# Kernel optimization log

Hardware: AMD Instinct MI355X
Metric: run time of the kernel (lower is better)

The kernel has to match this reference:

```python
import jax, jax.numpy as jnp
import numpy as np

B, L, D, T, S, K = 16, 4095, 768, 768, 64, 8
H = T // 2  # per-direction GRU hidden


def setup_inputs() -> dict:
    key = jax.random.key(0)
    ks = jax.random.split(key, 16)
    sc = 0.05
    hidden = jax.random.normal(ks[0], (B, L, D), jnp.float32)
    attn_len = jax.random.randint(ks[1], (B,), L // 2, L).astype(jnp.int32)
    span_start = jax.random.randint(ks[2], (B, S), 0, L - 16).astype(jnp.int32)
    span_len = jax.random.randint(ks[3], (B, S), 1, 9).astype(jnp.int32)
    return dict(
        hidden=hidden,
        W_ih_f=jax.random.normal(ks[4], (3 * H, D)) * sc,
        W_hh_f=jax.random.normal(ks[5], (3 * H, H)) * sc,
        b_ih_f=jax.random.normal(ks[6], (3 * H,)) * sc,
        b_hh_f=jax.random.normal(ks[7], (3 * H,)) * sc,
        W_ih_b=jax.random.normal(ks[8], (3 * H, D)) * sc,
        W_hh_b=jax.random.normal(ks[9], (3 * H, H)) * sc,
        b_ih_b=jax.random.normal(ks[10], (3 * H,)) * sc,
        b_hh_b=jax.random.normal(ks[11], (3 * H,)) * sc,
        W_ctx=jax.random.normal(ks[12], (T, D)) * sc,
        b_ctx=jax.random.normal(ks[13], (T,)) * sc,
        W_find=jax.random.normal(ks[14], (1, 2 * T)) * sc,
        attn_len=attn_len,
        span_start=span_start,
        span_len=span_len,
    )


def _gru_dir(x, W_ih, W_hh, b_ih, b_hh, reverse):
    # x: [B, S, D] -> [B, S, H]; torch GRU gate order: r, z, n
    def step(h, xt):
        gi = xt @ W_ih.T + b_ih            # [B, 3H]
        gh = h @ W_hh.T + b_hh
        ir, iz, inn = jnp.split(gi, 3, axis=-1)
        hr, hz, hn = jnp.split(gh, 3, axis=-1)
        r = jax.nn.sigmoid(ir + hr)
        z = jax.nn.sigmoid(iz + hz)
        n = jnp.tanh(inn + r * hn)
        h_new = (1.0 - z) * n + z * h
        return h_new, h_new
    xs = jnp.swapaxes(x, 0, 1)             # [S, B, D]
    h0 = jnp.zeros((x.shape[0], W_hh.shape[1]), x.dtype)
    _, ys = jax.lax.scan(step, h0, xs, reverse=reverse)
    return jnp.swapaxes(ys, 0, 1)          # [B, S, H]


def reference(hidden, W_ih_f, W_hh_f, b_ih_f, b_hh_f, W_ih_b, W_hh_b, b_ih_b, b_hh_b,
              W_ctx, b_ctx, W_find, attn_len, span_start, span_len):
    pos = jnp.arange(L)
    # --- per-span mean pooling (ragged spans, vectorized via masks) ---
    end = span_start + span_len - 1        # inclusive end, as hidden[start:end+1]
    mask = (pos[None, None, :] >= span_start[..., None]) & (pos[None, None, :] <= end[..., None])
    maskf = mask.astype(hidden.dtype)      # [B, S, L]
    cnt = maskf.sum(-1, keepdims=True)
    span_rep = jnp.einsum('bsl,bld->bsd', maskf, hidden) / cnt   # [B, S, D]
    # --- bidirectional GRU over the span sequence ---
    h_f = _gru_dir(span_rep, W_ih_f, W_hh_f, b_ih_f, b_hh_f, reverse=False)
    h_b = _gru_dir(span_rep, W_ih_b, W_hh_b, b_ih_b, b_hh_b, reverse=True)
    rep_ac = jnp.concatenate([h_f, h_b], axis=-1)                # [B, S, T]
    # --- context: mean over valid tokens excluding the last valid token, then linear ---
    n_ctx = (attn_len - 1).astype(hidden.dtype)                  # [B]
    ctx_mask = (pos[None, :] < (attn_len - 1)[:, None]).astype(hidden.dtype)
    ctx = jnp.einsum('bl,bld->bd', ctx_mask, hidden) / n_ctx[:, None]
    rep_context = ctx @ W_ctx.T + b_ctx                          # [B, T]
    # --- findm attention: concat + linear(no bias) + sigmoid + topk + gather ---
    all_reps = jnp.concatenate([rep_ac, rep_context[:, None, :]], axis=1)  # [B, S+1, T]
    wq, wk = W_find[0, :T], W_find[0, T:]
    # sigmoid(W [q; k]) = sigmoid(q.wq + k.wk)
    score = jax.nn.sigmoid((rep_ac @ wq)[:, :, None] + (all_reps @ wk)[:, None, :])  # [B, S, S+1]
    vals, idx = jax.lax.top_k(score, K)                          # [B, S, K]
    v1 = jnp.take_along_axis(all_reps[:, None, :, :], idx[..., None], axis=2)        # [B, S, K, T]
    return rep_ac, rep_context, v1, vals, idx
```

## Files before the change

### kernel.cpp

```cpp
#include <hip/hip_runtime.h>
#include <hip/hip_bf16.h>
#include <math.h>

#define BB 16
#define LL 4095
#define DD 768
#define TT 768
#define SS 64
#define KK 8
#define HH 384
#define G3 1152
#define NWPD 24

__global__ void span_mean_kernel(const float* __restrict__ hidden,
                                 const int* __restrict__ sstart,
                                 const int* __restrict__ slen,
                                 float* __restrict__ span) {
    int bs = blockIdx.x;
    int b = bs >> 6;
    int st = sstart[bs];
    int ln = slen[bs];
    const float* base = hidden + ((size_t)b * LL + st) * DD;
    float inv = 1.0f / (float)ln;
    for (int d = threadIdx.x; d < DD; d += 256) {
        float acc = 0.0f;
        for (int r = 0; r < ln; ++r) acc += base[(size_t)r * DD + d];
        span[(size_t)bs * DD + d] = acc * inv;
    }
}

__global__ void ctx_accum_kernel(const float* __restrict__ hidden,
                                 const int* __restrict__ attn_len,
                                 float* __restrict__ ctx) {
    int b = blockIdx.x, chunk = blockIdx.y;
    int lim = attn_len[b] - 1;
    int l0 = chunk * 128;
    int l1 = min(l0 + 128, lim);
    if (l0 >= l1) return;
    int t = threadIdx.x;
    const float* base = hidden + (size_t)b * LL * DD;
    float a0 = 0.f, a1 = 0.f, a2 = 0.f;
    for (int l = l0; l < l1; ++l) {
        const float* row = base + (size_t)l * DD;
        a0 += row[t]; a1 += row[t + 256]; a2 += row[t + 512];
    }
    atomicAdd(&ctx[b * DD + t], a0);
    atomicAdd(&ctx[b * DD + t + 256], a1);
    atomicAdd(&ctx[b * DD + t + 512], a2);
}

__global__ void repctx_kernel(const float* __restrict__ ctxsum,
                              const int* __restrict__ attn_len,
                              const float* __restrict__ W_ctx,
                              const float* __restrict__ b_ctx,
                              float* __restrict__ out_rc) {
    int b = blockIdx.x;
    int j = blockIdx.y * 256 + threadIdx.x;
    __shared__ float cv[DD];
    float inv = 1.0f / (float)(attn_len[b] - 1);
    for (int d = threadIdx.x; d < DD; d += 256) cv[d] = ctxsum[b * DD + d] * inv;
    __syncthreads();
    const float* wr = W_ctx + (size_t)j * DD;
    float acc = b_ctx[j];
    for (int d = 0; d < DD; ++d) acc += wr[d] * cv[d];
    out_rc[b * TT + j] = acc;
}

__global__ __launch_bounds__(256) void gi_gemm_kernel(
        const float* __restrict__ span,
        const float* __restrict__ Wf, const float* __restrict__ Wb,
        const float* __restrict__ bihf, const float* __restrict__ bhhf,
        const float* __restrict__ bihb, const float* __restrict__ bhhb,
        float* __restrict__ gi) {
    int dir = blockIdx.z;
    const float* W = dir ? Wb : Wf;
    const float* bih = dir ? bihb : bihf;
    const float* bhh = dir ? bhhb : bhhf;
    int m0 = blockIdx.x * 64, n0 = blockIdx.y * 64;
    __shared__ float As[64][17];
    __shared__ float Bs[64][17];
    int t = threadIdx.x, tx = t & 15, ty = t >> 4;
    float acc[4][4] = {{0.f}};
    for (int k0 = 0; k0 < DD; k0 += 16) {
        for (int e = t; e < 1024; e += 256) {
            int r = e >> 4, c = e & 15;
            As[r][c] = span[(size_t)(m0 + r) * DD + k0 + c];
            Bs[r][c] = W[(size_t)(n0 + r) * DD + k0 + c];
        }
        __syncthreads();
#pragma unroll
        for (int kk = 0; kk < 16; ++kk) {
            float a[4], bv[4];
#pragma unroll
            for (int i = 0; i < 4; ++i) a[i] = As[ty * 4 + i][kk];
#pragma unroll
            for (int j = 0; j < 4; ++j) bv[j] = Bs[tx * 4 + j][kk];
#pragma unroll
            for (int i = 0; i < 4; ++i)
#pragma unroll
                for (int j = 0; j < 4; ++j) acc[i][j] += a[i] * bv[j];
        }
        __syncthreads();
    }
#pragma unroll
    for (int i = 0; i < 4; ++i)
#pragma unroll
        for (int j = 0; j < 4; ++j) {
            int m = m0 + ty * 4 + i, n = n0 + tx * 4 + j;
            float v = acc[i][j] + bih[n] + (n < 2 * HH ? bhh[n] : 0.0f);
            gi[((size_t)dir * 1024 + m) * G3 + n] = v;
        }
}

__global__ __launch_bounds__(256, 1) void scan_coop_kernel(
        const float* __restrict__ gi,
        const float* __restrict__ Whf, const float* __restrict__ Whb,
        const float* __restrict__ bhhf, const float* __restrict__ bhhb,
        unsigned long long* __restrict__ hpair,
        float* __restrict__ repac) {
    int wg = blockIdx.x;
    int dir = wg / NWPD;
    int w = wg % NWPD;
    int t = threadIdx.x;
    int kseg = t & 15, i_loc = t >> 4;
    int i_glob = w * 16 + i_loc;
    const float* Wh = dir ? Whb : Whf;

    float4 wr[3][6];
#pragma unroll
    for (int g = 0; g < 3; ++g)
#pragma unroll
        for (int j = 0; j < 6; ++j) {
            wr[g][j] = *(const float4*)(Wh + (size_t)(g * HH + i_glob) * HH + kseg * 4 + 64 * j);
            asm volatile("" : "+v"(wr[g][j].x), "+v"(wr[g][j].y),
                              "+v"(wr[g][j].z), "+v"(wr[g][j].w));
        }
    float bhn = (dir ? bhhb : bhhf)[2 * HH + i_glob];

    __shared__ __align__(16) float hs[6144];
    float4* hs4 = (float4*)hs;

    for (int s = 0; s < 64; ++s) {
        int p = dir ? (63 - s) : s;
        const float* grow = gi + ((size_t)dir * 1024 + kseg * 64 + p) * G3;
        float g_r = grow[i_glob], g_z = grow[HH + i_glob], g_n = grow[2 * HH + i_glob];
        {
            const unsigned long long* src = hpair + (size_t)((s & 1) * 2 + dir) * 6144;
            unsigned int expect = (unsigned int)s;
            unsigned long long vals[24];
            for (;;) {
                bool ok = true;
#pragma unroll
                for (int j = 0; j < 24; ++j) {
                    vals[j] = __hip_atomic_load(src + j * 256 + t,
                                                __ATOMIC_RELAXED, __HIP_MEMORY_SCOPE_AGENT);
                    ok &= ((unsigned int)(vals[j] >> 32) == expect);
                }
                if (ok) break;
                __builtin_amdgcn_s_sleep(1);
            }
#pragma unroll
            for (int j = 0; j < 24; ++j)
                hs[j * 256 + t] = __uint_as_float((unsigned int)vals[j]);
        }
        __syncthreads();
        float pr[16], pz[16], pn[16];
#pragma unroll
        for (int b = 0; b < 16; ++b) {
            float4 hq[6];
#pragma unroll
            for (int j = 0; j < 6; ++j) hq[j] = hs4[b * 96 + kseg + 16 * j];
            float ar = 0.f, az = 0.f, an = 0.f;
#pragma unroll
            for (int j = 0; j < 6; ++j) {
                ar += wr[0][j].x * hq[j].x + wr[0][j].y * hq[j].y + wr[0][j].z * hq[j].z + wr[0][j].w * hq[j].w;
                az += wr[1][j].x * hq[j].x + wr[1][j].y * hq[j].y + wr[1][j].z * hq[j].z + wr[1][j].w * hq[j].w;
                an += wr[2][j].x * hq[j].x + wr[2][j].y * hq[j].y + wr[2][j].z * hq[j].z + wr[2][j].w * hq[j].w;
            }
            pr[b] = ar; pz[b] = az; pn[b] = an;
        }
        float qr[8], qz[8], qn[8];
        {
            const bool hi = (kseg & 8) != 0;
#pragma unroll
            for (int j = 0; j < 8; ++j) {
                float sr_ = hi ? pr[j] : pr[j + 8];
                qr[j] = (hi ? pr[j + 8] : pr[j]) + __shfl_xor(sr_, 8);
                float sz_ = hi ? pz[j] : pz[j + 8];
                qz[j] = (hi ? pz[j + 8] : pz[j]) + __shfl_xor(sz_, 8);
                float sn_ = hi ? pn[j] : pn[j + 8];
                qn[j] = (hi ? pn[j + 8] : pn[j]) + __shfl_xor(sn_, 8);
            }
        }
        float ur[4], uz[4], un[4];
        {
            const bool hi = (kseg & 4) != 0;
#pragma unroll
            for (int j = 0; j < 4; ++j) {
                float sr_ = hi ? qr[j] : qr[j + 4];
                ur[j] = (hi ? qr[j + 4] : qr[j]) + __shfl_xor(sr_, 4);
                float sz_ = hi ? qz[j] : qz[j + 4];
                uz[j] = (hi ? qz[j + 4] : qz[j]) + __shfl_xor(sz_, 4);
                float sn_ = hi ? qn[j] : qn[j + 4];
                un[j] = (hi ? qn[j + 4] : qn[j]) + __shfl_xor(sn_, 4);
            }
        }
        float vr[2], vz[2], vn[2];
        {
            const bool hi = (kseg & 2) != 0;
#pragma unroll
            for (int j = 0; j < 2; ++j) {
                float sr_ = hi ? ur[j] : ur[j + 2];
                vr[j] = (hi ? ur[j + 2] : ur[j]) + __shfl_xor(sr_, 2);
                float sz_ = hi ? uz[j] : uz[j + 2];
                vz[j] = (hi ? uz[j + 2] : uz[j]) + __shfl_xor(sz_, 2);
                float sn_ = hi ? un[j] : un[j + 2];
                vn[j] = (hi ? un[j + 2] : un[j]) + __shfl_xor(sn_, 2);
            }
        }
        float sr, sz, sn;
        {
            const bool hi = (kseg & 1) != 0;
            float sr_ = hi ? vr[0] : vr[1];
            sr = (hi ? vr[1] : vr[0]) + __shfl_xor(sr_, 1);
            float sz_ = hi ? vz[0] : vz[1];
            sz = (hi ? vz[1] : vz[0]) + __shfl_xor(sz_, 1);
            float sn_ = hi ? vn[0] : vn[1];
            sn = (hi ? vn[1] : vn[0]) + __shfl_xor(sn_, 1);
        }
        float r = 1.0f / (1.0f + expf(-(g_r + sr)));
        float z = 1.0f / (1.0f + expf(-(g_z + sz)));
        float n = tanhf(g_n + r * (sn + bhn));
        float hold = hs[kseg * 384 + i_glob];
        float hnew = (1.0f - z) * n + z * hold;
        unsigned long long pv = ((unsigned long long)(unsigned int)(s + 1) << 32)
                              | (unsigned long long)__float_as_uint(hnew);
        __hip_atomic_store(hpair + (size_t)(((s + 1) & 1) * 2 + dir) * 6144 + kseg * 384 + i_glob,
                           pv, __ATOMIC_RELAXED, __HIP_MEMORY_SCOPE_AGENT);
        repac[(size_t)(kseg * 64 + p) * TT + dir * HH + i_glob] = hnew;
        __syncthreads();
    }
}

__global__ void qkv_kernel(const float* __restrict__ repac,
                           const float* __restrict__ repctx,
                           const float* __restrict__ Wfind,
                           float* __restrict__ qv, float* __restrict__ kv) {
    int w = blockIdx.x * 4 + (threadIdx.x >> 6);
    int lane = threadIdx.x & 63;
    const float* row;
    const float* vec;
    float* dst;
    if (w < 1024) {
        row = repac + (size_t)w * TT;
        vec = Wfind;
        dst = qv + w;
    } else {
        int u = w - 1024;
        int b = u / 65, j = u % 65;
        row = (j < 64) ? (repac + (size_t)(b * 64 + j) * TT) : (repctx + (size_t)b * TT);
        vec = Wfind + TT;
        dst = kv + u;
    }
    double acc = 0.0;
    for (int d = lane; d < TT; d += 64) acc += (double)row[d] * (double)vec[d];
#pragma unroll
    for (int off = 32; off > 0; off >>= 1) acc += __shfl_down(acc, off);
    if (lane == 0) *dst = (float)acc;
}

__global__ void topk_kernel(const float* __restrict__ qv,
                            const float* __restrict__ kv,
                            float* __restrict__ vals_out,
                            float* __restrict__ idx_out,
                            int* __restrict__ idxw) {
    int t = threadIdx.x;
    int bs = blockIdx.x * 256 + t;
    int b = bs >> 6;
    int b0 = (blockIdx.x * 256) >> 6;
    __shared__ float kvs[4 * 65];
    for (int e = t; e < 4 * 65; e += 256) kvs[e] = kv[(b0 + e / 65) * 65 + e % 65];
    __syncthreads();
    const float* myk = kvs + (b - b0) * 65;
    float q = qv[bs];
    float sc[65];
#pragma unroll 1
    for (int j = 0; j < 65; ++j) {
        float x = q + myk[j];
        float e = (float)exp(-(double)x);
        sc[j] = 1.0f / (1.0f + e);
    }
    unsigned long long taken = 0ull;
    bool tk64 = false;
    for (int kk = 0; kk < 8; ++kk) {
        float best = -3.0e38f;
        int bj = 0;
        for (int j = 0; j < 65; ++j) {
            bool tkn = (j < 64) ? (((taken >> j) & 1ull) != 0ull) : tk64;
            float v = sc[j];
            if (!tkn && v > best) { best = v; bj = j; }
        }
        if (bj < 64) taken |= (1ull << bj); else tk64 = true;
        vals_out[bs * 8 + kk] = best;
        idx_out[bs * 8 + kk] = (float)bj;
        idxw[bs * 8 + kk] = bj;
    }
}

__global__ void v1_kernel(const float* __restrict__ repac,
                          const float* __restrict__ repctx,
                          const int* __restrict__ idxw,
                          float* __restrict__ v1) {
    int bs = blockIdx.x;
    int b = bs >> 6;
    int t = threadIdx.x;
    for (int kk = 0; kk < 8; ++kk) {
        int j = idxw[bs * 8 + kk];
        const float* src = (j < 64) ? (repac + (size_t)(b * 64 + j) * TT)
                                    : (repctx + (size_t)b * TT);
        float* dst = v1 + ((size_t)bs * 8 + kk) * TT;
        for (int d = t; d < DD; d += 256) dst[d] = src[d];
    }
}

extern "C" void kernel_launch(void* const* d_in, const int* in_sizes, int n_in,
                              void* d_out, int out_size, void* d_ws, size_t ws_size,
                              hipStream_t stream) {
    const float* hidden    = (const float*)d_in[0];
    const float* W_ih_f    = (const float*)d_in[1];
    const float* W_hh_f    = (const float*)d_in[2];
    const float* b_ih_f    = (const float*)d_in[3];
    const float* b_hh_f    = (const float*)d_in[4];
    const float* W_ih_b    = (const float*)d_in[5];
    const float* W_hh_b    = (const float*)d_in[6];
    const float* b_ih_b    = (const float*)d_in[7];
    const float* b_hh_b    = (const float*)d_in[8];
    const float* W_ctx     = (const float*)d_in[9];
    const float* b_ctx     = (const float*)d_in[10];
    const float* W_find    = (const float*)d_in[11];
    const int*   attn_len  = (const int*)d_in[12];
    const int*   span_start= (const int*)d_in[13];
    const int*   span_len  = (const int*)d_in[14];
    (void)in_sizes; (void)n_in; (void)out_size; (void)ws_size;

    float* ws   = (float*)d_ws;
    float* span = ws;
    float* gi   = span + 786432;
    float* ctx  = gi + 2359296;
    float* qv   = ctx + 12288;
    float* kv   = qv + 1024;
    int*   idxw = (int*)(kv + 1040);
    unsigned long long* hpair = (unsigned long long*)span;

    float* out      = (float*)d_out;
    float* o_repac  = out;
    float* o_repctx = out + 786432;
    float* o_v1     = out + 798720;
    float* o_vals   = out + 7090176;
    float* o_idx    = out + 7098368;

    hipMemsetAsync(ctx, 0, (size_t)BB * DD * sizeof(float), stream);

    span_mean_kernel<<<1024, 256, 0, stream>>>(hidden, span_start, span_len, span);
    ctx_accum_kernel<<<dim3(BB, 32), 256, 0, stream>>>(hidden, attn_len, ctx);
    repctx_kernel<<<dim3(BB, 3), 256, 0, stream>>>(ctx, attn_len, W_ctx, b_ctx, o_repctx);
    gi_gemm_kernel<<<dim3(16, 18, 2), 256, 0, stream>>>(span, W_ih_f, W_ih_b,
                                                        b_ih_f, b_hh_f, b_ih_b, b_hh_b, gi);
    hipMemsetAsync(hpair, 0, (size_t)24576 * sizeof(unsigned long long), stream);
    scan_coop_kernel<<<48, 256, 0, stream>>>(gi, W_hh_f, W_hh_b, b_hh_f, b_hh_b,
                                             hpair, o_repac);
    qkv_kernel<<<516, 256, 0, stream>>>(o_repac, o_repctx, W_find, qv, kv);
    topk_kernel<<<4, 256, 0, stream>>>(qv, kv, o_vals, o_idx, idxw);
    v1_kernel<<<1024, 256, 0, stream>>>(o_repac, o_repctx, idxw, o_v1);
}
```

Measured before the change: 947.8 us.

## Double-buffer scan hidden state, skip polling own slice, vectorize gi GEMM smem reads

The GRU scan kernel now keeps two LDS hidden-state buffers. Each workgroup writes its own new h slice straight into the next buffer and skips the global atomic polling for the entries it owns. This removes the trailing __syncthreads per step and cuts global spin-load traffic on the cross-workgroup critical path. Separately, the gi GEMM stores its shared tiles transposed (k-major), so each thread reads a float4 instead of four strided scalar loads. The risks are a race on the double buffer, since its correctness depends on the barrier after polling, and bank conflicts from the transposed tile stores.

```diff
diff --git a/kernel.cpp b/kernel.cpp
--- a/kernel.cpp
+++ b/kernel.cpp
@@ -77,24 +77,23 @@
     const float* bih = dir ? bihb : bihf;
     const float* bhh = dir ? bhhb : bhhf;
     int m0 = blockIdx.x * 64, n0 = blockIdx.y * 64;
-    __shared__ float As[64][17];
-    __shared__ float Bs[64][17];
+    __shared__ float As[16][68];
+    __shared__ float Bs[16][68];
     int t = threadIdx.x, tx = t & 15, ty = t >> 4;
     float acc[4][4] = {{0.f}};
     for (int k0 = 0; k0 < DD; k0 += 16) {
         for (int e = t; e < 1024; e += 256) {
             int r = e >> 4, c = e & 15;
-            As[r][c] = span[(size_t)(m0 + r) * DD + k0 + c];
-            Bs[r][c] = W[(size_t)(n0 + r) * DD + k0 + c];
+            As[c][r] = span[(size_t)(m0 + r) * DD + k0 + c];
+            Bs[c][r] = W[(size_t)(n0 + r) * DD + k0 + c];
         }
         __syncthreads();
 #pragma unroll
         for (int kk = 0; kk < 16; ++kk) {
-            float a[4], bv[4];
-#pragma unroll
-            for (int i = 0; i < 4; ++i) a[i] = As[ty * 4 + i][kk];
-#pragma unroll
-            for (int j = 0; j < 4; ++j) bv[j] = Bs[tx * 4 + j][kk];
+            float4 a4 = *(const float4*)&As[kk][ty * 4];
+            float4 b4 = *(const float4*)&Bs[kk][tx * 4];
+            float a[4] = {a4.x, a4.y, a4.z, a4.w};
+            float bv[4] = {b4.x, b4.y, b4.z, b4.w};
 #pragma unroll
             for (int i = 0; i < 4; ++i)
 #pragma unroll
@@ -137,31 +136,38 @@
         }
     float bhn = (dir ? bhhb : bhhf)[2 * HH + i_glob];
 
-    __shared__ __align__(16) float hs[6144];
-    float4* hs4 = (float4*)hs;
+    __shared__ __align__(16) float hsbuf[2][6144];
+
+    unsigned ownmask = 0u;
+#pragma unroll
+    for (int j = 0; j < 24; ++j)
+        if ((((j * 256 + t) % 384) >> 4) == w) ownmask |= (1u << j);
+
+    hsbuf[0][kseg * 384 + i_glob] = 0.0f;
 
     for (int s = 0; s < 64; ++s) {
+        float* hs  = hsbuf[s & 1];
+        float* hsN = hsbuf[(s + 1) & 1];
+        const float4* hs4 = (const float4*)hs;
         int p = dir ? (63 - s) : s;
         const float* grow = gi + ((size_t)dir * 1024 + kseg * 64 + p) * G3;
         float g_r = grow[i_glob], g_z = grow[HH + i_glob], g_n = grow[2 * HH + i_glob];
         {
             const unsigned long long* src = hpair + (size_t)((s & 1) * 2 + dir) * 6144;
             unsigned int expect = (unsigned int)s;
-            unsigned long long vals[24];
             for (;;) {
                 bool ok = true;
 #pragma unroll
                 for (int j = 0; j < 24; ++j) {
-                    vals[j] = __hip_atomic_load(src + j * 256 + t,
+                    if ((ownmask >> j) & 1u) continue;
+                    unsigned long long v = __hip_atomic_load(src + j * 256 + t,
                                                 __ATOMIC_RELAXED, __HIP_MEMORY_SCOPE_AGENT);
-                    ok &= ((unsigned int)(vals[j] >> 32) == expect);
+                    hs[j * 256 + t] = __uint_as_float((unsigned int)v);
+                    ok &= ((unsigned int)(v >> 32) == expect);
                 }
                 if (ok) break;
                 __builtin_amdgcn_s_sleep(1);
             }
-#pragma unroll
-            for (int j = 0; j < 24; ++j)
-                hs[j * 256 + t] = __uint_as_float((unsigned int)vals[j]);
         }
         __syncthreads();
         float pr[16], pz[16], pn[16];
@@ -233,12 +239,12 @@
         float n = tanhf(g_n + r * (sn + bhn));
         float hold = hs[kseg * 384 + i_glob];
         float hnew = (1.0f - z) * n + z * hold;
+        hsN[kseg * 384 + i_glob] = hnew;
         unsigned long long pv = ((unsigned long long)(unsigned int)(s + 1) << 32)
                               | (unsigned long long)__float_as_uint(hnew);
         __hip_atomic_store(hpair + (size_t)(((s + 1) & 1) * 2 + dir) * 6144 + kseg * 384 + i_glob,
                            pv, __ATOMIC_RELAXED, __HIP_MEMORY_SCOPE_AGENT);
         repac[(size_t)(kseg * 64 + p) * TT + dir * HH + i_glob] = hnew;
-        __syncthreads();
     }
 }
 
```

New measurement: 1.393 ms. +46.9%, slower.
